# Kernel optimization log

Hardware: AMD Instinct MI355X
Metric: run time of the kernel (lower is better)

The kernel has to match this reference:

```python
import jax, jax.numpy as jnp
import numpy as np

B, S, D, H = 512, 512, 64, 128  # batch, seq_len, input_size, hidden_size


def setup_inputs() -> dict:
    key = jax.random.key(0)
    ks = jax.random.split(key, 12)
    s_in = 1.0 / np.sqrt(H)
    def u(k, shape):
        return jax.random.uniform(k, shape, jnp.float32, -s_in, s_in)
    return {
        "x": jax.random.normal(ks[0], (B, S, D), jnp.float32),
        # layer 0 (PyTorch gate order i,f,g,o stacked along first dim)
        "W_ih0": u(ks[1], (4 * H, D)),
        "W_hh0": u(ks[2], (4 * H, H)),
        "b_ih0": u(ks[3], (4 * H,)),
        "b_hh0": u(ks[4], (4 * H,)),
        # layer 1
        "W_ih1": u(ks[5], (4 * H, H)),
        "W_hh1": u(ks[6], (4 * H, H)),
        "b_ih1": u(ks[7], (4 * H,)),
        "b_hh1": u(ks[8], (4 * H,)),
        # linear head hidden -> 1
        "W_lin": u(ks[9], (1, H)),
        "b_lin": u(ks[10], (1,)),
    }


def _lstm_layer(x, W_ih, W_hh, b_ih, b_hh):
    # x: [B, S, Din] -> h sequence [B, S, H]
    b, s, _ = x.shape
    h_dim = W_hh.shape[1]
    # precompute input contribution for all timesteps (the compute-heavy GEMM)
    pre = jnp.einsum('bsd,gd->bsg', x, W_ih) + (b_ih + b_hh)  # [B, S, 4H]

    def step(carry, p_t):
        h, c = carry
        gates = p_t + h @ W_hh.T  # [B, 4H]
        i, f, g, o = jnp.split(gates, 4, axis=-1)
        i = jax.nn.sigmoid(i)
        f = jax.nn.sigmoid(f)
        g = jnp.tanh(g)
        o = jax.nn.sigmoid(o)
        c = f * c + i * g
        h = o * jnp.tanh(c)
        return (h, c), h

    h0 = jnp.zeros((b, h_dim), x.dtype)
    (_, _), hs = jax.lax.scan(step, (h0, h0), pre.transpose(1, 0, 2))
    return hs.transpose(1, 0, 2)  # [B, S, H]


def reference(x, W_ih0, W_hh0, b_ih0, b_hh0, W_ih1, W_hh1, b_ih1, b_hh1, W_lin, b_lin):
    h1 = _lstm_layer(x, W_ih0, W_hh0, b_ih0, b_hh0)
    h2 = _lstm_layer(h1, W_ih1, W_hh1, b_ih1, b_hh1)
    last = h2[:, -1, :]  # [B, H]
    return last @ W_lin.T + b_lin  # [B, 1]
```

## Files before the change

### kernel.cpp

```cpp
#include <hip/hip_runtime.h>

typedef _Float16 half8 __attribute__((ext_vector_type(8)));
typedef _Float16 half4 __attribute__((ext_vector_type(4)));
typedef _Float16 half2v __attribute__((ext_vector_type(2)));
typedef float floatx4 __attribute__((ext_vector_type(4)));

__device__ __forceinline__ float fast_rcp(float x) { return __builtin_amdgcn_rcpf(x); }
__device__ __forceinline__ float fast_sigmoid(float x) {
  return fast_rcp(1.f + __expf(-x));
}
__device__ __forceinline__ float fast_tanh(float x) {
  return 1.f - 2.f * fast_rcp(1.f + __expf(2.f * x));
}

__global__ void prep_kernel(const float* __restrict__ wih0, const float* __restrict__ whh0,
                            const float* __restrict__ bih0, const float* __restrict__ bhh0,
                            const float* __restrict__ wih1, const float* __restrict__ whh1,
                            const float* __restrict__ bih1, const float* __restrict__ bhh1,
                            _Float16* __restrict__ w0f, _Float16* __restrict__ w1f,
                            float* __restrict__ bias0, float* __restrict__ bias1)
{
  int stride = gridDim.x * blockDim.x;
  int idx0 = blockIdx.x * blockDim.x + threadIdx.x;
  const int N0 = 6*32*64*8;
  const int N1 = 8*32*64*8;
  for (int e = idx0; e < N0 + N1 + 1024; e += stride) {
    if (e < N0) {
      int j = e & 7; int le = e >> 3; int lane = le & 63; int frag = le >> 6;
      int kt = frag >> 5, ntile = frag & 31;
      int n = ntile*16 + (lane & 15);
      int kk = kt*32 + ((lane >> 4) << 3) + j;
      float v = (kk < 64) ? wih0[n*64 + kk] : whh0[n*128 + (kk - 64)];
      w0f[e] = (_Float16)v;
    } else if (e < N0 + N1) {
      int e2 = e - N0;
      int j = e2 & 7; int le = e2 >> 3; int lane = le & 63; int frag = le >> 6;
      int kt = frag >> 5, ntile = frag & 31;
      int n = ntile*16 + (lane & 15);
      int kk = kt*32 + ((lane >> 4) << 3) + j;
      float v = (kk < 128) ? wih1[n*128 + kk] : whh1[n*128 + (kk - 128)];
      w1f[e2] = (_Float16)v;
    } else {
      int i = e - (N0 + N1);
      if (i < 512) bias0[i] = bih0[i] + bhh0[i];
      else         bias1[i - 512] = bih1[i - 512] + bhh1[i - 512];
    }
  }
}


__global__ __launch_bounds__(512, 2) void lstm_l0(const float* __restrict__ x,
    const _Float16* __restrict__ w0f, const float* __restrict__ bias0,
    _Float16* __restrict__ h1out)
{
  const int tid = threadIdx.x;
  const int lane = tid & 63;
  const int w = tid >> 6;
  const int r0 = blockIdx.x * 2;

  __shared__ float preLDS[2][8192];
  __shared__ half8 aF[2][2*64];
  __shared__ half8 hA[2][4*8];
  __shared__ _Float16 hist[16][2][128];

  for (int i = tid; i < 2*4*8*4; i += 512) ((int*)hA)[i] = 0;

  half8 bf[6][4];
#pragma unroll
  for (int kt = 0; kt < 6; ++kt)
#pragma unroll
    for (int g = 0; g < 4; ++g) {
      int frag = kt*32 + (g*8 + w);
      bf[kt][g] = *reinterpret_cast<const half8*>(w0f + (size_t)(frag*64 + lane)*8);
      asm volatile("" : "+a"(bf[kt][g]));
    }
  float bias_v[4];
#pragma unroll
  for (int g = 0; g < 4; ++g) bias_v[g] = bias0[g*128 + w*16 + (lane & 15)];

  const int sdt = tid >> 6, sr = (tid >> 5) & 1, scp = (tid & 31) * 2;
  const int sm = sdt*2 + sr;
  const int sidx = ((scp>>5)*64 + sm + (((scp&31)>>3)<<4))*8 + (scp & 7);

  const bool arow = (lane & 11) == 0;
  const int cIdx = ((lane >> 4) << 1) | ((lane >> 2) & 1);
  const int rb = lane >> 4;
  const int en = w*16 + (lane & 15);
  const int eoff = ((en>>5)*8 + ((en&31)>>3)*2 + rb)*8 + (en&7);
  float cst = 0.f;

  {
    float2 v0 = *reinterpret_cast<const float2*>(x + ((size_t)(r0+sr)*512 + sdt)*64 + scp);
    float2 v1 = *reinterpret_cast<const float2*>(x + ((size_t)(r0+sr)*512 + 8 + sdt)*64 + scp);
    half2v h0; h0[0] = (_Float16)v0.x; h0[1] = (_Float16)v0.y;
    half2v h1v; h1v[0] = (_Float16)v1.x; h1v[1] = (_Float16)v1.y;
    *reinterpret_cast<half2v*>(((_Float16*)aF[0]) + sidx) = h0;
    *reinterpret_cast<half2v*>(((_Float16*)aF[1]) + sidx) = h1v;
  }
  __syncthreads();
  {
    floatx4 accP[4];
#pragma unroll
    for (int g = 0; g < 4; ++g) { float bb = bias_v[g]; accP[g] = (floatx4){bb,bb,bb,bb}; }
#pragma unroll
    for (int kt = 0; kt < 2; ++kt) {
      half8 af = aF[0][kt*64 + lane];
#pragma unroll
      for (int g = 0; g < 4; ++g)
        accP[g] = __builtin_amdgcn_mfma_f32_16x16x32_f16(af, bf[kt][g], accP[g], 0, 0, 0);
    }
#pragma unroll
    for (int reg = 0; reg < 4; ++reg) {
      int m = ((lane>>4)<<2) + reg;
      floatx4 pv = (floatx4){accP[0][reg], accP[1][reg], accP[2][reg], accP[3][reg]};
      *reinterpret_cast<floatx4*>(&preLDS[0][(m*128 + en)*4]) = pv;
    }
  }
  __syncthreads();

  half8 a2 = {}, a3 = {}, a4 = {}, a5 = {};

  for (int t = 0; t < 512; ++t) {
    const int b = t >> 3;
    if ((t & 7) == 0 && b < 62) {
      int s = (b+2)*8 + sdt;
      float2 v = *reinterpret_cast<const float2*>(x + ((size_t)(r0+sr)*512 + s)*64 + scp);
      half2v hv; hv[0] = (_Float16)v.x; hv[1] = (_Float16)v.y;
      *reinterpret_cast<half2v*>(((_Float16*)aF[b&1]) + sidx) = hv;
    }
    __syncthreads();
    if ((t & 7) == 0) {
      if (t != 0) {
        int tbase = t - 8;
        int fr = tid >> 8, rest = tid & 255;
        int fdt = rest >> 5, n = (rest & 31) * 4;
        half4 v = *reinterpret_cast<const half4*>(&hist[(tbase + fdt) & 15][fr][n]);
        *reinterpret_cast<half4*>(h1out + ((size_t)(r0 + fr)*512 + tbase + fdt)*128 + n) = v;
      }
      if (b < 63) {
        int slot = (b+1) & 1;
        floatx4 accP[4];
#pragma unroll
        for (int g = 0; g < 4; ++g) { float bb = bias_v[g]; accP[g] = (floatx4){bb,bb,bb,bb}; }
#pragma unroll
        for (int kt = 0; kt < 2; ++kt) {
          half8 af = aF[slot][kt*64 + lane];
#pragma unroll
          for (int g = 0; g < 4; ++g)
            accP[g] = __builtin_amdgcn_mfma_f32_16x16x32_f16(af, bf[kt][g], accP[g], 0, 0, 0);
        }
#pragma unroll
        for (int reg = 0; reg < 4; ++reg) {
          int m = ((lane>>4)<<2) + reg;
          floatx4 pv = (floatx4){accP[0][reg], accP[1][reg], accP[2][reg], accP[3][reg]};
          *reinterpret_cast<floatx4*>(&preLDS[slot][(m*128 + en)*4]) = pv;
        }
      }
    }

    floatx4 p4 = (floatx4){0.f, 0.f, 0.f, 0.f};
    if (lane < 32) {
      int mstep = ((t & 7) << 1) + rb;
      p4 = *reinterpret_cast<const floatx4*>(&preLDS[b & 1][(mstep*128 + en)*4]);
    }
    floatx4 acc[4];
#pragma unroll
    for (int g = 0; g < 4; ++g) acc[g] = (floatx4){p4[g], 0.f, 0.f, 0.f};

    const int cur = t & 1;
    if (arow) {
      a2 = hA[cur][0*8 + cIdx];
      a3 = hA[cur][1*8 + cIdx];
      a4 = hA[cur][2*8 + cIdx];
      a5 = hA[cur][3*8 + cIdx];
    }
#pragma unroll
    for (int g = 0; g < 4; ++g)
      acc[g] = __builtin_amdgcn_mfma_f32_16x16x32_f16(a2, bf[2][g], acc[g], 0, 0, 0);
#pragma unroll
    for (int g = 0; g < 4; ++g)
      acc[g] = __builtin_amdgcn_mfma_f32_16x16x32_f16(a3, bf[3][g], acc[g], 0, 0, 0);
#pragma unroll
    for (int g = 0; g < 4; ++g)
      acc[g] = __builtin_amdgcn_mfma_f32_16x16x32_f16(a4, bf[4][g], acc[g], 0, 0, 0);
#pragma unroll
    for (int g = 0; g < 4; ++g)
      acc[g] = __builtin_amdgcn_mfma_f32_16x16x32_f16(a5, bf[5][g], acc[g], 0, 0, 0);

    if (lane < 32) {
      float ii = fast_sigmoid(acc[0][0]);
      float ff = fast_sigmoid(acc[1][0]);
      float gg = fast_tanh(acc[2][0]);
      float oo = fast_sigmoid(acc[3][0]);
      cst = ff*cst + ii*gg;
      float hv2 = oo*fast_tanh(cst);
      _Float16 hh = (_Float16)hv2;
      ((_Float16*)hA[cur^1])[eoff] = hh;
      hist[t & 15][rb][en] = hh;
    }
  }
  __syncthreads();
  {
    int tbase = 504;
    int fr = tid >> 8, rest = tid & 255;
    int fdt = rest >> 5, n = (rest & 31) * 4;
    half4 v = *reinterpret_cast<const half4*>(&hist[(tbase + fdt) & 15][fr][n]);
    *reinterpret_cast<half4*>(h1out + ((size_t)(r0 + fr)*512 + tbase + fdt)*128 + n) = v;
  }
}

__global__ __launch_bounds__(512, 2) void lstm_l1(const _Float16* __restrict__ h1in,
    const _Float16* __restrict__ w1f, const float* __restrict__ bias1,
    const float* __restrict__ wlin, const float* __restrict__ blin,
    float* __restrict__ out)
{
  const int tid = threadIdx.x;
  const int lane = tid & 63;
  const int w = tid >> 6;
  const int r0 = blockIdx.x * 2;

  __shared__ float preLDS[2][8192];
  __shared__ half8 aF[2][4*64];
  __shared__ half8 hA[2][4*8];
  __shared__ float head[256];

  for (int i = tid; i < 2*4*8*4; i += 512) ((int*)hA)[i] = 0;

  half8 bf[8][4];
#pragma unroll
  for (int kt = 0; kt < 8; ++kt)
#pragma unroll
    for (int g = 0; g < 4; ++g) {
      int frag = kt*32 + (g*8 + w);
      bf[kt][g] = *reinterpret_cast<const half8*>(w1f + (size_t)(frag*64 + lane)*8);
      asm volatile("" : "+a"(bf[kt][g]));
    }
  float bias_v[4];
#pragma unroll
  for (int g = 0; g < 4; ++g) bias_v[g] = bias1[g*128 + w*16 + (lane & 15)];

  const int sdt = tid >> 6, sr = (tid >> 5) & 1, scq = (tid & 31) * 4;
  const int sm = sdt*2 + sr;
  const int sidx = ((scq>>5)*64 + sm + (((scq&31)>>3)<<4))*8 + (scq & 7);

  const bool arow = (lane & 11) == 0;
  const int cIdx = ((lane >> 4) << 1) | ((lane >> 2) & 1);
  const int rb = lane >> 4;
  const int en = w*16 + (lane & 15);
  const int eoff = ((en>>5)*8 + ((en&31)>>3)*2 + rb)*8 + (en&7);
  const float wl = (lane < 32) ? wlin[en] : 0.f;
  float cst = 0.f;
  float hl = 0.f;

  {
    uint2 v0 = *reinterpret_cast<const uint2*>(h1in + ((size_t)(r0+sr)*512 + sdt)*128 + scq);
    uint2 v1 = *reinterpret_cast<const uint2*>(h1in + ((size_t)(r0+sr)*512 + 8 + sdt)*128 + scq);
    *reinterpret_cast<uint2*>(((_Float16*)aF[0]) + sidx) = v0;
    *reinterpret_cast<uint2*>(((_Float16*)aF[1]) + sidx) = v1;
  }
  __syncthreads();
  {
    floatx4 accP[4];
#pragma unroll
    for (int g = 0; g < 4; ++g) { float bb = bias_v[g]; accP[g] = (floatx4){bb,bb,bb,bb}; }
#pragma unroll
    for (int kt = 0; kt < 4; ++kt) {
      half8 af = aF[0][kt*64 + lane];
#pragma unroll
      for (int g = 0; g < 4; ++g)
        accP[g] = __builtin_amdgcn_mfma_f32_16x16x32_f16(af, bf[kt][g], accP[g], 0, 0, 0);
    }
#pragma unroll
    for (int reg = 0; reg < 4; ++reg) {
      int m = ((lane>>4)<<2) + reg;
      floatx4 pv = (floatx4){accP[0][reg], accP[1][reg], accP[2][reg], accP[3][reg]};
      *reinterpret_cast<floatx4*>(&preLDS[0][(m*128 + en)*4]) = pv;
    }
  }
  __syncthreads();

  half8 a4 = {}, a5 = {}, a6 = {}, a7 = {};

  for (int t = 0; t < 512; ++t) {
    const int b = t >> 3;
    if ((t & 7) == 0 && b < 62) {
      int s = (b+2)*8 + sdt;
      uint2 v = *reinterpret_cast<const uint2*>(h1in + ((size_t)(r0+sr)*512 + s)*128 + scq);
      *reinterpret_cast<uint2*>(((_Float16*)aF[b&1]) + sidx) = v;
    }
    __syncthreads();
    if ((t & 7) == 0 && b < 63) {
      int slot = (b+1) & 1;
      floatx4 accP[4];
#pragma unroll
      for (int g = 0; g < 4; ++g) { float bb = bias_v[g]; accP[g] = (floatx4){bb,bb,bb,bb}; }
#pragma unroll
      for (int kt = 0; kt < 4; ++kt) {
        half8 af = aF[slot][kt*64 + lane];
#pragma unroll
        for (int g = 0; g < 4; ++g)
          accP[g] = __builtin_amdgcn_mfma_f32_16x16x32_f16(af, bf[kt][g], accP[g], 0, 0, 0);
      }
#pragma unroll
      for (int reg = 0; reg < 4; ++reg) {
        int m = ((lane>>4)<<2) + reg;
        floatx4 pv = (floatx4){accP[0][reg], accP[1][reg], accP[2][reg], accP[3][reg]};
        *reinterpret_cast<floatx4*>(&preLDS[slot][(m*128 + en)*4]) = pv;
      }
    }

    floatx4 p4 = (floatx4){0.f, 0.f, 0.f, 0.f};
    if (lane < 32) {
      int mstep = ((t & 7) << 1) + rb;
      p4 = *reinterpret_cast<const floatx4*>(&preLDS[b & 1][(mstep*128 + en)*4]);
    }
    floatx4 acc[4];
#pragma unroll
    for (int g = 0; g < 4; ++g) acc[g] = (floatx4){p4[g], 0.f, 0.f, 0.f};

    const int cur = t & 1;
    if (arow) {
      a4 = hA[cur][0*8 + cIdx];
      a5 = hA[cur][1*8 + cIdx];
      a6 = hA[cur][2*8 + cIdx];
      a7 = hA[cur][3*8 + cIdx];
    }
#pragma unroll
    for (int g = 0; g < 4; ++g)
      acc[g] = __builtin_amdgcn_mfma_f32_16x16x32_f16(a4, bf[4][g], acc[g], 0, 0, 0);
#pragma unroll
    for (int g = 0; g < 4; ++g)
      acc[g] = __builtin_amdgcn_mfma_f32_16x16x32_f16(a5, bf[5][g], acc[g], 0, 0, 0);
#pragma unroll
    for (int g = 0; g < 4; ++g)
      acc[g] = __builtin_amdgcn_mfma_f32_16x16x32_f16(a6, bf[6][g], acc[g], 0, 0, 0);
#pragma unroll
    for (int g = 0; g < 4; ++g)
      acc[g] = __builtin_amdgcn_mfma_f32_16x16x32_f16(a7, bf[7][g], acc[g], 0, 0, 0);

    if (lane < 32) {
      float ii = fast_sigmoid(acc[0][0]);
      float ff = fast_sigmoid(acc[1][0]);
      float gg = fast_tanh(acc[2][0]);
      float oo = fast_sigmoid(acc[3][0]);
      cst = ff*cst + ii*gg;
      hl = oo*fast_tanh(cst);
      ((_Float16*)hA[cur^1])[eoff] = (_Float16)hl;
    }
  }

  if (lane < 32) head[rb*128 + en] = hl * wl;
  __syncthreads();
  if (tid < 2) {
    float s = blin[0];
    for (int n = 0; n < 128; ++n) s += head[tid*128 + n];
    out[r0 + tid] = s;
  }
}

extern "C" void kernel_launch(void* const* d_in, const int* in_sizes, int n_in,
                              void* d_out, int out_size, void* d_ws, size_t ws_size,
                              hipStream_t stream)
{
  const float* x    = (const float*)d_in[0];
  const float* wih0 = (const float*)d_in[1];
  const float* whh0 = (const float*)d_in[2];
  const float* bih0 = (const float*)d_in[3];
  const float* bhh0 = (const float*)d_in[4];
  const float* wih1 = (const float*)d_in[5];
  const float* whh1 = (const float*)d_in[6];
  const float* bih1 = (const float*)d_in[7];
  const float* bhh1 = (const float*)d_in[8];
  const float* wlin = (const float*)d_in[9];
  const float* blin = (const float*)d_in[10];
  float* out = (float*)d_out;

  char* ws = (char*)d_ws;
  _Float16* w0f = (_Float16*)(ws);
  _Float16* w1f = (_Float16*)(ws + 196608);
  float* bias0  = (float*)(ws + 458752);
  float* bias1  = (float*)(ws + 460800);
  _Float16* h1  = (_Float16*)(ws + 1048576);

  prep_kernel<<<256, 256, 0, stream>>>(wih0, whh0, bih0, bhh0, wih1, whh1, bih1, bhh1,
                                       w0f, w1f, bias0, bias1);
  lstm_l0<<<256, 512, 0, stream>>>(x, w0f, bias0, h1);
  lstm_l1<<<256, 512, 0, stream>>>(h1, w1f, bias1, wlin, blin, out);
}
```

Measured before the change: 785.2 us.

## Fuse both LSTM layers into one wavefront-pipelined kernel

Merges the layer-0 and layer-1 kernels into a single kernel that runs layer 1 sixteen timesteps behind layer 0. Layer-0 outputs pass through an LDS history ring instead of a global h1 buffer. This removes the global round trip of h1 and the second launch, and lets the two recurrences interleave to hide latency. To fit registers, only the recurrent weights stay resident; the input-projection weights are reloaded from global memory every 8 steps. The cost is higher register and LDS pressure and a longer serial step per iteration.

```diff
diff --git a/kernel.cpp b/kernel.cpp
--- a/kernel.cpp
+++ b/kernel.cpp
@@ -48,168 +48,8 @@
   }
 }
 
-
-__global__ __launch_bounds__(512, 2) void lstm_l0(const float* __restrict__ x,
+__global__ __launch_bounds__(512, 2) void lstm_fused(const float* __restrict__ x,
     const _Float16* __restrict__ w0f, const float* __restrict__ bias0,
-    _Float16* __restrict__ h1out)
-{
-  const int tid = threadIdx.x;
-  const int lane = tid & 63;
-  const int w = tid >> 6;
-  const int r0 = blockIdx.x * 2;
-
-  __shared__ float preLDS[2][8192];
-  __shared__ half8 aF[2][2*64];
-  __shared__ half8 hA[2][4*8];
-  __shared__ _Float16 hist[16][2][128];
-
-  for (int i = tid; i < 2*4*8*4; i += 512) ((int*)hA)[i] = 0;
-
-  half8 bf[6][4];
-#pragma unroll
-  for (int kt = 0; kt < 6; ++kt)
-#pragma unroll
-    for (int g = 0; g < 4; ++g) {
-      int frag = kt*32 + (g*8 + w);
-      bf[kt][g] = *reinterpret_cast<const half8*>(w0f + (size_t)(frag*64 + lane)*8);
-      asm volatile("" : "+a"(bf[kt][g]));
-    }
-  float bias_v[4];
-#pragma unroll
-  for (int g = 0; g < 4; ++g) bias_v[g] = bias0[g*128 + w*16 + (lane & 15)];
-
-  const int sdt = tid >> 6, sr = (tid >> 5) & 1, scp = (tid & 31) * 2;
-  const int sm = sdt*2 + sr;
-  const int sidx = ((scp>>5)*64 + sm + (((scp&31)>>3)<<4))*8 + (scp & 7);
-
-  const bool arow = (lane & 11) == 0;
-  const int cIdx = ((lane >> 4) << 1) | ((lane >> 2) & 1);
-  const int rb = lane >> 4;
-  const int en = w*16 + (lane & 15);
-  const int eoff = ((en>>5)*8 + ((en&31)>>3)*2 + rb)*8 + (en&7);
-  float cst = 0.f;
-
-  {
-    float2 v0 = *reinterpret_cast<const float2*>(x + ((size_t)(r0+sr)*512 + sdt)*64 + scp);
-    float2 v1 = *reinterpret_cast<const float2*>(x + ((size_t)(r0+sr)*512 + 8 + sdt)*64 + scp);
-    half2v h0; h0[0] = (_Float16)v0.x; h0[1] = (_Float16)v0.y;
-    half2v h1v; h1v[0] = (_Float16)v1.x; h1v[1] = (_Float16)v1.y;
-    *reinterpret_cast<half2v*>(((_Float16*)aF[0]) + sidx) = h0;
-    *reinterpret_cast<half2v*>(((_Float16*)aF[1]) + sidx) = h1v;
-  }
-  __syncthreads();
-  {
-    floatx4 accP[4];
-#pragma unroll
-    for (int g = 0; g < 4; ++g) { float bb = bias_v[g]; accP[g] = (floatx4){bb,bb,bb,bb}; }
-#pragma unroll
-    for (int kt = 0; kt < 2; ++kt) {
-      half8 af = aF[0][kt*64 + lane];
-#pragma unroll
-      for (int g = 0; g < 4; ++g)
-        accP[g] = __builtin_amdgcn_mfma_f32_16x16x32_f16(af, bf[kt][g], accP[g], 0, 0, 0);
-    }
-#pragma unroll
-    for (int reg = 0; reg < 4; ++reg) {
-      int m = ((lane>>4)<<2) + reg;
-      floatx4 pv = (floatx4){accP[0][reg], accP[1][reg], accP[2][reg], accP[3][reg]};
-      *reinterpret_cast<floatx4*>(&preLDS[0][(m*128 + en)*4]) = pv;
-    }
-  }
-  __syncthreads();
-
-  half8 a2 = {}, a3 = {}, a4 = {}, a5 = {};
-
-  for (int t = 0; t < 512; ++t) {
-    const int b = t >> 3;
-    if ((t & 7) == 0 && b < 62) {
-      int s = (b+2)*8 + sdt;
-      float2 v = *reinterpret_cast<const float2*>(x + ((size_t)(r0+sr)*512 + s)*64 + scp);
-      half2v hv; hv[0] = (_Float16)v.x; hv[1] = (_Float16)v.y;
-      *reinterpret_cast<half2v*>(((_Float16*)aF[b&1]) + sidx) = hv;
-    }
-    __syncthreads();
-    if ((t & 7) == 0) {
-      if (t != 0) {
-        int tbase = t - 8;
-        int fr = tid >> 8, rest = tid & 255;
-        int fdt = rest >> 5, n = (rest & 31) * 4;
-        half4 v = *reinterpret_cast<const half4*>(&hist[(tbase + fdt) & 15][fr][n]);
-        *reinterpret_cast<half4*>(h1out + ((size_t)(r0 + fr)*512 + tbase + fdt)*128 + n) = v;
-      }
-      if (b < 63) {
-        int slot = (b+1) & 1;
-        floatx4 accP[4];
-#pragma unroll
-        for (int g = 0; g < 4; ++g) { float bb = bias_v[g]; accP[g] = (floatx4){bb,bb,bb,bb}; }
-#pragma unroll
-        for (int kt = 0; kt < 2; ++kt) {
-          half8 af = aF[slot][kt*64 + lane];
-#pragma unroll
-          for (int g = 0; g < 4; ++g)
-            accP[g] = __builtin_amdgcn_mfma_f32_16x16x32_f16(af, bf[kt][g], accP[g], 0, 0, 0);
-        }
-#pragma unroll
-        for (int reg = 0; reg < 4; ++reg) {
-          int m = ((lane>>4)<<2) + reg;
-          floatx4 pv = (floatx4){accP[0][reg], accP[1][reg], accP[2][reg], accP[3][reg]};
-          *reinterpret_cast<floatx4*>(&preLDS[slot][(m*128 + en)*4]) = pv;
-        }
-      }
-    }
-
-    floatx4 p4 = (floatx4){0.f, 0.f, 0.f, 0.f};
-    if (lane < 32) {
-      int mstep = ((t & 7) << 1) + rb;
-      p4 = *reinterpret_cast<const floatx4*>(&preLDS[b & 1][(mstep*128 + en)*4]);
-    }
-    floatx4 acc[4];
-#pragma unroll
-    for (int g = 0; g < 4; ++g) acc[g] = (floatx4){p4[g], 0.f, 0.f, 0.f};
-
-    const int cur = t & 1;
-    if (arow) {
-      a2 = hA[cur][0*8 + cIdx];
-      a3 = hA[cur][1*8 + cIdx];
-      a4 = hA[cur][2*8 + cIdx];
-      a5 = hA[cur][3*8 + cIdx];
-    }
-#pragma unroll
-    for (int g = 0; g < 4; ++g)
-      acc[g] = __builtin_amdgcn_mfma_f32_16x16x32_f16(a2, bf[2][g], acc[g], 0, 0, 0);
-#pragma unroll
-    for (int g = 0; g < 4; ++g)
-      acc[g] = __builtin_amdgcn_mfma_f32_16x16x32_f16(a3, bf[3][g], acc[g], 0, 0, 0);
-#pragma unroll
-    for (int g = 0; g < 4; ++g)
-      acc[g] = __builtin_amdgcn_mfma_f32_16x16x32_f16(a4, bf[4][g], acc[g], 0, 0, 0);
-#pragma unroll
-    for (int g = 0; g < 4; ++g)
-      acc[g] = __builtin_amdgcn_mfma_f32_16x16x32_f16(a5, bf[5][g], acc[g], 0, 0, 0);
-
-    if (lane < 32) {
-      float ii = fast_sigmoid(acc[0][0]);
-      float ff = fast_sigmoid(acc[1][0]);
-      float gg = fast_tanh(acc[2][0]);
-      float oo = fast_sigmoid(acc[3][0]);
-      cst = ff*cst + ii*gg;
-      float hv2 = oo*fast_tanh(cst);
-      _Float16 hh = (_Float16)hv2;
-      ((_Float16*)hA[cur^1])[eoff] = hh;
-      hist[t & 15][rb][en] = hh;
-    }
-  }
-  __syncthreads();
-  {
-    int tbase = 504;
-    int fr = tid >> 8, rest = tid & 255;
-    int fdt = rest >> 5, n = (rest & 31) * 4;
-    half4 v = *reinterpret_cast<const half4*>(&hist[(tbase + fdt) & 15][fr][n]);
-    *reinterpret_cast<half4*>(h1out + ((size_t)(r0 + fr)*512 + tbase + fdt)*128 + n) = v;
-  }
-}
-
-__global__ __launch_bounds__(512, 2) void lstm_l1(const _Float16* __restrict__ h1in,
     const _Float16* __restrict__ w1f, const float* __restrict__ bias1,
     const float* __restrict__ wlin, const float* __restrict__ blin,
     float* __restrict__ out)
@@ -219,29 +59,36 @@
   const int w = tid >> 6;
   const int r0 = blockIdx.x * 2;
 
-  __shared__ float preLDS[2][8192];
-  __shared__ half8 aF[2][4*64];
-  __shared__ half8 hA[2][4*8];
+  __shared__ float pre0[2][8192];
+  __shared__ float pre1[2][8192];
+  __shared__ half8 aF[2][2*64];
+  __shared__ half8 hA0[2][4*8];
+  __shared__ half8 hA1[2][4*8];
+  __shared__ _Float16 hist[16][2][128];
   __shared__ float head[256];
 
-  for (int i = tid; i < 2*4*8*4; i += 512) ((int*)hA)[i] = 0;
-
-  half8 bf[8][4];
-#pragma unroll
-  for (int kt = 0; kt < 8; ++kt)
+  if (tid < 256) { ((int*)hA0)[tid] = 0; ((int*)hA1)[tid] = 0; }
+
+  half8 bf0r[4][4], bf1r[4][4];
+#pragma unroll
+  for (int kt = 0; kt < 4; ++kt)
 #pragma unroll
     for (int g = 0; g < 4; ++g) {
-      int frag = kt*32 + (g*8 + w);
-      bf[kt][g] = *reinterpret_cast<const half8*>(w1f + (size_t)(frag*64 + lane)*8);
-      asm volatile("" : "+a"(bf[kt][g]));
-    }
-  float bias_v[4];
-#pragma unroll
-  for (int g = 0; g < 4; ++g) bias_v[g] = bias1[g*128 + w*16 + (lane & 15)];
-
-  const int sdt = tid >> 6, sr = (tid >> 5) & 1, scq = (tid & 31) * 4;
+      bf0r[kt][g] = *reinterpret_cast<const half8*>(w0f + (size_t)(((kt+2)*32 + g*8 + w)*64 + lane)*8);
+      asm volatile("" : "+a"(bf0r[kt][g]));
+      bf1r[kt][g] = *reinterpret_cast<const half8*>(w1f + (size_t)(((kt+4)*32 + g*8 + w)*64 + lane)*8);
+      asm volatile("" : "+a"(bf1r[kt][g]));
+    }
+  float b0v[4], b1v[4];
+#pragma unroll
+  for (int g = 0; g < 4; ++g) {
+    b0v[g] = bias0[g*128 + w*16 + (lane & 15)];
+    b1v[g] = bias1[g*128 + w*16 + (lane & 15)];
+  }
+
+  const int sdt = tid >> 6, sr = (tid >> 5) & 1, scp = (tid & 31) * 2;
   const int sm = sdt*2 + sr;
-  const int sidx = ((scq>>5)*64 + sm + (((scq&31)>>3)<<4))*8 + (scq & 7);
+  const int sidx = ((scp>>5)*64 + sm + (((scp&31)>>3)<<4))*8 + (scp & 7);
 
   const bool arow = (lane & 11) == 0;
   const int cIdx = ((lane >> 4) << 1) | ((lane >> 2) & 1);
@@ -249,103 +96,189 @@
   const int en = w*16 + (lane & 15);
   const int eoff = ((en>>5)*8 + ((en&31)>>3)*2 + rb)*8 + (en&7);
   const float wl = (lane < 32) ? wlin[en] : 0.f;
-  float cst = 0.f;
-  float hl = 0.f;
+  float cst0 = 0.f, cst1 = 0.f, hl = 0.f;
+
+  const int dtL = (lane & 15) >> 1;
+  const int rL  = lane & 1;
+  const int kbase = (lane >> 4) * 8;
 
   {
-    uint2 v0 = *reinterpret_cast<const uint2*>(h1in + ((size_t)(r0+sr)*512 + sdt)*128 + scq);
-    uint2 v1 = *reinterpret_cast<const uint2*>(h1in + ((size_t)(r0+sr)*512 + 8 + sdt)*128 + scq);
-    *reinterpret_cast<uint2*>(((_Float16*)aF[0]) + sidx) = v0;
-    *reinterpret_cast<uint2*>(((_Float16*)aF[1]) + sidx) = v1;
+    float2 v0 = *reinterpret_cast<const float2*>(x + ((size_t)(r0+sr)*512 + sdt)*64 + scp);
+    float2 v1 = *reinterpret_cast<const float2*>(x + ((size_t)(r0+sr)*512 + 8 + sdt)*64 + scp);
+    half2v h0; h0[0] = (_Float16)v0.x; h0[1] = (_Float16)v0.y;
+    half2v h1v; h1v[0] = (_Float16)v1.x; h1v[1] = (_Float16)v1.y;
+    *reinterpret_cast<half2v*>(((_Float16*)aF[0]) + sidx) = h0;
+    *reinterpret_cast<half2v*>(((_Float16*)aF[1]) + sidx) = h1v;
   }
   __syncthreads();
   {
     floatx4 accP[4];
 #pragma unroll
-    for (int g = 0; g < 4; ++g) { float bb = bias_v[g]; accP[g] = (floatx4){bb,bb,bb,bb}; }
-#pragma unroll
-    for (int kt = 0; kt < 4; ++kt) {
+    for (int g = 0; g < 4; ++g) { float bb = b0v[g]; accP[g] = (floatx4){bb,bb,bb,bb}; }
+#pragma unroll
+    for (int kt = 0; kt < 2; ++kt) {
       half8 af = aF[0][kt*64 + lane];
 #pragma unroll
-      for (int g = 0; g < 4; ++g)
-        accP[g] = __builtin_amdgcn_mfma_f32_16x16x32_f16(af, bf[kt][g], accP[g], 0, 0, 0);
+      for (int g = 0; g < 4; ++g) {
+        half8 wf = *reinterpret_cast<const half8*>(w0f + (size_t)((kt*32 + g*8 + w)*64 + lane)*8);
+        accP[g] = __builtin_amdgcn_mfma_f32_16x16x32_f16(af, wf, accP[g], 0, 0, 0);
+      }
     }
 #pragma unroll
     for (int reg = 0; reg < 4; ++reg) {
       int m = ((lane>>4)<<2) + reg;
       floatx4 pv = (floatx4){accP[0][reg], accP[1][reg], accP[2][reg], accP[3][reg]};
-      *reinterpret_cast<floatx4*>(&preLDS[0][(m*128 + en)*4]) = pv;
+      *reinterpret_cast<floatx4*>(&pre0[0][(m*128 + en)*4]) = pv;
     }
   }
   __syncthreads();
 
-  half8 a4 = {}, a5 = {}, a6 = {}, a7 = {};
-
-  for (int t = 0; t < 512; ++t) {
-    const int b = t >> 3;
-    if ((t & 7) == 0 && b < 62) {
+  half8 a00 = {}, a01 = {}, a02 = {}, a03 = {};
+  half8 a10 = {}, a11 = {}, a12 = {}, a13 = {};
+
+  for (int p = 0; p < 528; ++p) {
+    const int b = p >> 3;
+    if ((p & 7) == 0 && b < 62) {
       int s = (b+2)*8 + sdt;
-      uint2 v = *reinterpret_cast<const uint2*>(h1in + ((size_t)(r0+sr)*512 + s)*128 + scq);
-      *reinterpret_cast<uint2*>(((_Float16*)aF[b&1]) + sidx) = v;
+      float2 v = *reinterpret_cast<const float2*>(x + ((size_t)(r0+sr)*512 + s)*64 + scp);
+      half2v hv; hv[0] = (_Float16)v.x; hv[1] = (_Float16)v.y;
+      *reinterpret_cast<half2v*>(((_Float16*)aF[b&1]) + sidx) = hv;
     }
     __syncthreads();
-    if ((t & 7) == 0 && b < 63) {
-      int slot = (b+1) & 1;
-      floatx4 accP[4];
-#pragma unroll
-      for (int g = 0; g < 4; ++g) { float bb = bias_v[g]; accP[g] = (floatx4){bb,bb,bb,bb}; }
-#pragma unroll
-      for (int kt = 0; kt < 4; ++kt) {
-        half8 af = aF[slot][kt*64 + lane];
-#pragma unroll
-        for (int g = 0; g < 4; ++g)
-          accP[g] = __builtin_amdgcn_mfma_f32_16x16x32_f16(af, bf[kt][g], accP[g], 0, 0, 0);
-      }
-#pragma unroll
-      for (int reg = 0; reg < 4; ++reg) {
-        int m = ((lane>>4)<<2) + reg;
-        floatx4 pv = (floatx4){accP[0][reg], accP[1][reg], accP[2][reg], accP[3][reg]};
-        *reinterpret_cast<floatx4*>(&preLDS[slot][(m*128 + en)*4]) = pv;
-      }
-    }
-
-    floatx4 p4 = (floatx4){0.f, 0.f, 0.f, 0.f};
-    if (lane < 32) {
-      int mstep = ((t & 7) << 1) + rb;
-      p4 = *reinterpret_cast<const floatx4*>(&preLDS[b & 1][(mstep*128 + en)*4]);
-    }
-    floatx4 acc[4];
-#pragma unroll
-    for (int g = 0; g < 4; ++g) acc[g] = (floatx4){p4[g], 0.f, 0.f, 0.f};
-
-    const int cur = t & 1;
-    if (arow) {
-      a4 = hA[cur][0*8 + cIdx];
-      a5 = hA[cur][1*8 + cIdx];
-      a6 = hA[cur][2*8 + cIdx];
-      a7 = hA[cur][3*8 + cIdx];
-    }
-#pragma unroll
-    for (int g = 0; g < 4; ++g)
-      acc[g] = __builtin_amdgcn_mfma_f32_16x16x32_f16(a4, bf[4][g], acc[g], 0, 0, 0);
-#pragma unroll
-    for (int g = 0; g < 4; ++g)
-      acc[g] = __builtin_amdgcn_mfma_f32_16x16x32_f16(a5, bf[5][g], acc[g], 0, 0, 0);
-#pragma unroll
-    for (int g = 0; g < 4; ++g)
-      acc[g] = __builtin_amdgcn_mfma_f32_16x16x32_f16(a6, bf[6][g], acc[g], 0, 0, 0);
-#pragma unroll
-    for (int g = 0; g < 4; ++g)
-      acc[g] = __builtin_amdgcn_mfma_f32_16x16x32_f16(a7, bf[7][g], acc[g], 0, 0, 0);
-
-    if (lane < 32) {
-      float ii = fast_sigmoid(acc[0][0]);
-      float ff = fast_sigmoid(acc[1][0]);
-      float gg = fast_tanh(acc[2][0]);
-      float oo = fast_sigmoid(acc[3][0]);
-      cst = ff*cst + ii*gg;
-      hl = oo*fast_tanh(cst);
-      ((_Float16*)hA[cur^1])[eoff] = (_Float16)hl;
+
+    if ((p & 7) == 0) {
+      const _Float16* w0p = w0f; asm volatile("" : "+v"(w0p));
+      const _Float16* w1p = w1f; asm volatile("" : "+v"(w1p));
+      if (b < 63) {
+        int slot = (b+1) & 1;
+        floatx4 accP[4];
+#pragma unroll
+        for (int g = 0; g < 4; ++g) { float bb2 = b0v[g]; accP[g] = (floatx4){bb2,bb2,bb2,bb2}; }
+#pragma unroll
+        for (int kt = 0; kt < 2; ++kt) {
+          half8 af = aF[slot][kt*64 + lane];
+#pragma unroll
+          for (int g = 0; g < 4; ++g) {
+            half8 wf = *reinterpret_cast<const half8*>(w0p + (size_t)((kt*32 + g*8 + w)*64 + lane)*8);
+            accP[g] = __builtin_amdgcn_mfma_f32_16x16x32_f16(af, wf, accP[g], 0, 0, 0);
+          }
+        }
+#pragma unroll
+        for (int reg = 0; reg < 4; ++reg) {
+          int m = ((lane>>4)<<2) + reg;
+          floatx4 pv = (floatx4){accP[0][reg], accP[1][reg], accP[2][reg], accP[3][reg]};
+          *reinterpret_cast<floatx4*>(&pre0[slot][(m*128 + en)*4]) = pv;
+        }
+      }
+      int bb = b - 1;
+      if (bb >= 0 && bb < 64) {
+        int slot = bb & 1;
+        const _Float16* hrow = &hist[(bb & 1)*8 + dtL][rL][kbase];
+        floatx4 accP[4];
+#pragma unroll
+        for (int g = 0; g < 4; ++g) { float bb2 = b1v[g]; accP[g] = (floatx4){bb2,bb2,bb2,bb2}; }
+#pragma unroll
+        for (int kt = 0; kt < 4; ++kt) {
+          half8 af = *reinterpret_cast<const half8*>(hrow + kt*32);
+#pragma unroll
+          for (int g = 0; g < 4; ++g) {
+            half8 wf = *reinterpret_cast<const half8*>(w1p + (size_t)((kt*32 + g*8 + w)*64 + lane)*8);
+            accP[g] = __builtin_amdgcn_mfma_f32_16x16x32_f16(af, wf, accP[g], 0, 0, 0);
+          }
+        }
+#pragma unroll
+        for (int reg = 0; reg < 4; ++reg) {
+          int m = ((lane>>4)<<2) + reg;
+          floatx4 pv = (floatx4){accP[0][reg], accP[1][reg], accP[2][reg], accP[3][reg]};
+          *reinterpret_cast<floatx4*>(&pre1[slot][(m*128 + en)*4]) = pv;
+        }
+      }
+    }
+
+    if (p < 512) {
+      floatx4 p4 = (floatx4){0.f, 0.f, 0.f, 0.f};
+      if (lane < 32) {
+        int mstep = ((p & 7) << 1) + rb;
+        p4 = *reinterpret_cast<const floatx4*>(&pre0[b & 1][(mstep*128 + en)*4]);
+      }
+      floatx4 acc[4];
+#pragma unroll
+      for (int g = 0; g < 4; ++g) acc[g] = (floatx4){p4[g], 0.f, 0.f, 0.f};
+
+      const int cur = p & 1;
+      if (arow) {
+        a00 = hA0[cur][0*8 + cIdx];
+        a01 = hA0[cur][1*8 + cIdx];
+        a02 = hA0[cur][2*8 + cIdx];
+        a03 = hA0[cur][3*8 + cIdx];
+      }
+#pragma unroll
+      for (int g = 0; g < 4; ++g)
+        acc[g] = __builtin_amdgcn_mfma_f32_16x16x32_f16(a00, bf0r[0][g], acc[g], 0, 0, 0);
+#pragma unroll
+      for (int g = 0; g < 4; ++g)
+        acc[g] = __builtin_amdgcn_mfma_f32_16x16x32_f16(a01, bf0r[1][g], acc[g], 0, 0, 0);
+#pragma unroll
+      for (int g = 0; g < 4; ++g)
+        acc[g] = __builtin_amdgcn_mfma_f32_16x16x32_f16(a02, bf0r[2][g], acc[g], 0, 0, 0);
+#pragma unroll
+      for (int g = 0; g < 4; ++g)
+        acc[g] = __builtin_amdgcn_mfma_f32_16x16x32_f16(a03, bf0r[3][g], acc[g], 0, 0, 0);
+
+      if (lane < 32) {
+        float ii = fast_sigmoid(acc[0][0]);
+        float ff = fast_sigmoid(acc[1][0]);
+        float gg = fast_tanh(acc[2][0]);
+        float oo = fast_sigmoid(acc[3][0]);
+        cst0 = ff*cst0 + ii*gg;
+        float hv2 = oo*fast_tanh(cst0);
+        _Float16 hh = (_Float16)hv2;
+        ((_Float16*)hA0[cur^1])[eoff] = hh;
+        hist[p & 15][rb][en] = hh;
+      }
+    }
+
+    if (p >= 16) {
+      const int t1 = p - 16;
+      const int b1 = t1 >> 3;
+      floatx4 p4 = (floatx4){0.f, 0.f, 0.f, 0.f};
+      if (lane < 32) {
+        int mstep = ((t1 & 7) << 1) + rb;
+        p4 = *reinterpret_cast<const floatx4*>(&pre1[b1 & 1][(mstep*128 + en)*4]);
+      }
+      floatx4 acc[4];
+#pragma unroll
+      for (int g = 0; g < 4; ++g) acc[g] = (floatx4){p4[g], 0.f, 0.f, 0.f};
+
+      const int cur = t1 & 1;
+      if (arow) {
+        a10 = hA1[cur][0*8 + cIdx];
+        a11 = hA1[cur][1*8 + cIdx];
+        a12 = hA1[cur][2*8 + cIdx];
+        a13 = hA1[cur][3*8 + cIdx];
+      }
+#pragma unroll
+      for (int g = 0; g < 4; ++g)
+        acc[g] = __builtin_amdgcn_mfma_f32_16x16x32_f16(a10, bf1r[0][g], acc[g], 0, 0, 0);
+#pragma unroll
+      for (int g = 0; g < 4; ++g)
+        acc[g] = __builtin_amdgcn_mfma_f32_16x16x32_f16(a11, bf1r[1][g], acc[g], 0, 0, 0);
+#pragma unroll
+      for (int g = 0; g < 4; ++g)
+        acc[g] = __builtin_amdgcn_mfma_f32_16x16x32_f16(a12, bf1r[2][g], acc[g], 0, 0, 0);
+#pragma unroll
+      for (int g = 0; g < 4; ++g)
+        acc[g] = __builtin_amdgcn_mfma_f32_16x16x32_f16(a13, bf1r[3][g], acc[g], 0, 0, 0);
+
+      if (lane < 32) {
+        float ii = fast_sigmoid(acc[0][0]);
+        float ff = fast_sigmoid(acc[1][0]);
+        float gg = fast_tanh(acc[2][0]);
+        float oo = fast_sigmoid(acc[3][0]);
+        cst1 = ff*cst1 + ii*gg;
+        hl = oo*fast_tanh(cst1);
+        ((_Float16*)hA1[cur^1])[eoff] = (_Float16)hl;
+      }
     }
   }
 
@@ -380,10 +313,8 @@
   _Float16* w1f = (_Float16*)(ws + 196608);
   float* bias0  = (float*)(ws + 458752);
   float* bias1  = (float*)(ws + 460800);
-  _Float16* h1  = (_Float16*)(ws + 1048576);
 
   prep_kernel<<<256, 256, 0, stream>>>(wih0, whh0, bih0, bhh0, wih1, whh1, bih1, bhh1,
                                        w0f, w1f, bias0, bias1);
-  lstm_l0<<<256, 512, 0, stream>>>(x, w0f, bias0, h1);
-  lstm_l1<<<256, 512, 0, stream>>>(h1, w1f, bias1, wlin, blin, out);
-}
+  lstm_fused<<<256, 512, 0, stream>>>(x, w0f, bias0, w1f, bias1, wlin, blin, out);
+}
```

Result: slower. 889.3 us (+13.3%).

## Spread per-block prefetch, input GEMM and history stores across timestep phases

Applied to the files above, without the earlier changes.

The work that used to run every eighth timestep (global load of the next input chunk, the input-projection MFMAs and the history write-back) is now split across several phases of the 8-step block. The global load is issued at phase 0 and consumed at phase 1, and the projection is split over phases 2 and 3. The preactivation for the next step is read from LDS right after the recurrent MFMAs, so its latency is off the critical path. This is meant to smooth out the per-step latency spikes of the serial recurrence, at the cost of more live registers and phase-dependent branches.

```diff
diff --git a/kernel.cpp b/kernel.cpp
--- a/kernel.cpp
+++ b/kernel.cpp
@@ -48,7 +48,6 @@
   }
 }
 
-
 __global__ __launch_bounds__(512, 2) void lstm_l0(const float* __restrict__ x,
     const _Float16* __restrict__ w0f, const float* __restrict__ bias0,
     _Float16* __restrict__ h1out)
@@ -99,73 +98,78 @@
   }
   __syncthreads();
   {
-    floatx4 accP[4];
-#pragma unroll
-    for (int g = 0; g < 4; ++g) { float bb = bias_v[g]; accP[g] = (floatx4){bb,bb,bb,bb}; }
+    floatx4 accP0[4];
+#pragma unroll
+    for (int g = 0; g < 4; ++g) { float bb = bias_v[g]; accP0[g] = (floatx4){bb,bb,bb,bb}; }
 #pragma unroll
     for (int kt = 0; kt < 2; ++kt) {
       half8 af = aF[0][kt*64 + lane];
 #pragma unroll
       for (int g = 0; g < 4; ++g)
-        accP[g] = __builtin_amdgcn_mfma_f32_16x16x32_f16(af, bf[kt][g], accP[g], 0, 0, 0);
+        accP0[g] = __builtin_amdgcn_mfma_f32_16x16x32_f16(af, bf[kt][g], accP0[g], 0, 0, 0);
     }
 #pragma unroll
     for (int reg = 0; reg < 4; ++reg) {
       int m = ((lane>>4)<<2) + reg;
-      floatx4 pv = (floatx4){accP[0][reg], accP[1][reg], accP[2][reg], accP[3][reg]};
+      floatx4 pv = (floatx4){accP0[0][reg], accP0[1][reg], accP0[2][reg], accP0[3][reg]};
       *reinterpret_cast<floatx4*>(&preLDS[0][(m*128 + en)*4]) = pv;
     }
   }
-  __syncthreads();
 
   half8 a2 = {}, a3 = {}, a4 = {}, a5 = {};
+  float2 sv;
+  floatx4 accP[4];
+  floatx4 acc[4];
+#pragma unroll
+  for (int g = 0; g < 4; ++g) { acc[g] = (floatx4){0.f,0.f,0.f,0.f}; accP[g] = acc[g]; }
+
+  floatx4 p4c = (floatx4){0.f,0.f,0.f,0.f};
+  if (lane < 32)
+    p4c = *reinterpret_cast<const floatx4*>(&preLDS[0][(rb*128 + en)*4]);
 
   for (int t = 0; t < 512; ++t) {
     const int b = t >> 3;
-    if ((t & 7) == 0 && b < 62) {
+    __syncthreads();
+    const int ph = t & 7;
+    if (ph == 0 && b < 62) {
       int s = (b+2)*8 + sdt;
-      float2 v = *reinterpret_cast<const float2*>(x + ((size_t)(r0+sr)*512 + s)*64 + scp);
-      half2v hv; hv[0] = (_Float16)v.x; hv[1] = (_Float16)v.y;
+      sv = *reinterpret_cast<const float2*>(x + ((size_t)(r0+sr)*512 + s)*64 + scp);
+    }
+    if (ph == 1 && b < 62) {
+      half2v hv; hv[0] = (_Float16)sv.x; hv[1] = (_Float16)sv.y;
       *reinterpret_cast<half2v*>(((_Float16*)aF[b&1]) + sidx) = hv;
     }
-    __syncthreads();
-    if ((t & 7) == 0) {
-      if (t != 0) {
-        int tbase = t - 8;
-        int fr = tid >> 8, rest = tid & 255;
-        int fdt = rest >> 5, n = (rest & 31) * 4;
-        half4 v = *reinterpret_cast<const half4*>(&hist[(tbase + fdt) & 15][fr][n]);
-        *reinterpret_cast<half4*>(h1out + ((size_t)(r0 + fr)*512 + tbase + fdt)*128 + n) = v;
+    if (ph == 2 && b < 63) {
+      int slot = (b+1) & 1;
+#pragma unroll
+      for (int g = 0; g < 4; ++g) { float bb = bias_v[g]; accP[g] = (floatx4){bb,bb,bb,bb}; }
+      half8 af = aF[slot][lane];
+#pragma unroll
+      for (int g = 0; g < 4; ++g)
+        accP[g] = __builtin_amdgcn_mfma_f32_16x16x32_f16(af, bf[0][g], accP[g], 0, 0, 0);
+    }
+    if (ph == 3 && b < 63) {
+      int slot = (b+1) & 1;
+      half8 af = aF[slot][64 + lane];
+#pragma unroll
+      for (int g = 0; g < 4; ++g)
+        accP[g] = __builtin_amdgcn_mfma_f32_16x16x32_f16(af, bf[1][g], accP[g], 0, 0, 0);
+#pragma unroll
+      for (int reg = 0; reg < 4; ++reg) {
+        int m = ((lane>>4)<<2) + reg;
+        floatx4 pv = (floatx4){accP[0][reg], accP[1][reg], accP[2][reg], accP[3][reg]};
+        *reinterpret_cast<floatx4*>(&preLDS[slot][(m*128 + en)*4]) = pv;
       }
-      if (b < 63) {
-        int slot = (b+1) & 1;
-        floatx4 accP[4];
-#pragma unroll
-        for (int g = 0; g < 4; ++g) { float bb = bias_v[g]; accP[g] = (floatx4){bb,bb,bb,bb}; }
-#pragma unroll
-        for (int kt = 0; kt < 2; ++kt) {
-          half8 af = aF[slot][kt*64 + lane];
-#pragma unroll
-          for (int g = 0; g < 4; ++g)
-            accP[g] = __builtin_amdgcn_mfma_f32_16x16x32_f16(af, bf[kt][g], accP[g], 0, 0, 0);
-        }
-#pragma unroll
-        for (int reg = 0; reg < 4; ++reg) {
-          int m = ((lane>>4)<<2) + reg;
-          floatx4 pv = (floatx4){accP[0][reg], accP[1][reg], accP[2][reg], accP[3][reg]};
-          *reinterpret_cast<floatx4*>(&preLDS[slot][(m*128 + en)*4]) = pv;
-        }
-      }
-    }
-
-    floatx4 p4 = (floatx4){0.f, 0.f, 0.f, 0.f};
-    if (lane < 32) {
-      int mstep = ((t & 7) << 1) + rb;
-      p4 = *reinterpret_cast<const floatx4*>(&preLDS[b & 1][(mstep*128 + en)*4]);
-    }
-    floatx4 acc[4];
-#pragma unroll
-    for (int g = 0; g < 4; ++g) acc[g] = (floatx4){p4[g], 0.f, 0.f, 0.f};
+    }
+    if (ph == 5 && t >= 13) {
+      int tbase = t - 13;
+      int fr = tid >> 8, rest = tid & 255;
+      int fdt = rest >> 5, n = (rest & 31) * 4;
+      half4 v = *reinterpret_cast<const half4*>(&hist[(tbase + fdt) & 15][fr][n]);
+      *reinterpret_cast<half4*>(h1out + ((size_t)(r0 + fr)*512 + tbase + fdt)*128 + n) = v;
+    }
+
+    acc[0][0] = p4c[0]; acc[1][0] = p4c[1]; acc[2][0] = p4c[2]; acc[3][0] = p4c[3];
 
     const int cur = t & 1;
     if (arow) {
@@ -186,6 +190,12 @@
 #pragma unroll
     for (int g = 0; g < 4; ++g)
       acc[g] = __builtin_amdgcn_mfma_f32_16x16x32_f16(a5, bf[5][g], acc[g], 0, 0, 0);
+
+    if (lane < 32 && t < 511) {
+      int tn = t + 1;
+      int mstep = ((tn & 7) << 1) + rb;
+      p4c = *reinterpret_cast<const floatx4*>(&preLDS[(tn >> 3) & 1][(mstep*128 + en)*4]);
+    }
 
     if (lane < 32) {
       float ii = fast_sigmoid(acc[0][0]);
@@ -260,42 +270,62 @@
   }
   __syncthreads();
   {
-    floatx4 accP[4];
-#pragma unroll
-    for (int g = 0; g < 4; ++g) { float bb = bias_v[g]; accP[g] = (floatx4){bb,bb,bb,bb}; }
+    floatx4 accP0[4];
+#pragma unroll
+    for (int g = 0; g < 4; ++g) { float bb = bias_v[g]; accP0[g] = (floatx4){bb,bb,bb,bb}; }
 #pragma unroll
     for (int kt = 0; kt < 4; ++kt) {
       half8 af = aF[0][kt*64 + lane];
 #pragma unroll
       for (int g = 0; g < 4; ++g)
-        accP[g] = __builtin_amdgcn_mfma_f32_16x16x32_f16(af, bf[kt][g], accP[g], 0, 0, 0);
+        accP0[g] = __builtin_amdgcn_mfma_f32_16x16x32_f16(af, bf[kt][g], accP0[g], 0, 0, 0);
     }
 #pragma unroll
     for (int reg = 0; reg < 4; ++reg) {
       int m = ((lane>>4)<<2) + reg;
-      floatx4 pv = (floatx4){accP[0][reg], accP[1][reg], accP[2][reg], accP[3][reg]};
+      floatx4 pv = (floatx4){accP0[0][reg], accP0[1][reg], accP0[2][reg], accP0[3][reg]};
       *reinterpret_cast<floatx4*>(&preLDS[0][(m*128 + en)*4]) = pv;
     }
   }
-  __syncthreads();
 
   half8 a4 = {}, a5 = {}, a6 = {}, a7 = {};
+  uint2 sv;
+  floatx4 accP[4];
+  floatx4 acc[4];
+#pragma unroll
+  for (int g = 0; g < 4; ++g) { acc[g] = (floatx4){0.f,0.f,0.f,0.f}; accP[g] = acc[g]; }
+
+  floatx4 p4c = (floatx4){0.f,0.f,0.f,0.f};
+  if (lane < 32)
+    p4c = *reinterpret_cast<const floatx4*>(&preLDS[0][(rb*128 + en)*4]);
 
   for (int t = 0; t < 512; ++t) {
     const int b = t >> 3;
-    if ((t & 7) == 0 && b < 62) {
+    __syncthreads();
+    const int ph = t & 7;
+    if (ph == 0 && b < 62) {
       int s = (b+2)*8 + sdt;
-      uint2 v = *reinterpret_cast<const uint2*>(h1in + ((size_t)(r0+sr)*512 + s)*128 + scq);
-      *reinterpret_cast<uint2*>(((_Float16*)aF[b&1]) + sidx) = v;
-    }
-    __syncthreads();
-    if ((t & 7) == 0 && b < 63) {
+      sv = *reinterpret_cast<const uint2*>(h1in + ((size_t)(r0+sr)*512 + s)*128 + scq);
+    }
+    if (ph == 1 && b < 62) {
+      *reinterpret_cast<uint2*>(((_Float16*)aF[b&1]) + sidx) = sv;
+    }
+    if (ph == 2 && b < 63) {
       int slot = (b+1) & 1;
-      floatx4 accP[4];
 #pragma unroll
       for (int g = 0; g < 4; ++g) { float bb = bias_v[g]; accP[g] = (floatx4){bb,bb,bb,bb}; }
 #pragma unroll
-      for (int kt = 0; kt < 4; ++kt) {
+      for (int kt = 0; kt < 2; ++kt) {
+        half8 af = aF[slot][kt*64 + lane];
+#pragma unroll
+        for (int g = 0; g < 4; ++g)
+          accP[g] = __builtin_amdgcn_mfma_f32_16x16x32_f16(af, bf[kt][g], accP[g], 0, 0, 0);
+      }
+    }
+    if (ph == 3 && b < 63) {
+      int slot = (b+1) & 1;
+#pragma unroll
+      for (int kt = 2; kt < 4; ++kt) {
         half8 af = aF[slot][kt*64 + lane];
 #pragma unroll
         for (int g = 0; g < 4; ++g)
@@ -309,14 +339,7 @@
       }
     }
 
-    floatx4 p4 = (floatx4){0.f, 0.f, 0.f, 0.f};
-    if (lane < 32) {
-      int mstep = ((t & 7) << 1) + rb;
-      p4 = *reinterpret_cast<const floatx4*>(&preLDS[b & 1][(mstep*128 + en)*4]);
-    }
-    floatx4 acc[4];
-#pragma unroll
-    for (int g = 0; g < 4; ++g) acc[g] = (floatx4){p4[g], 0.f, 0.f, 0.f};
+    acc[0][0] = p4c[0]; acc[1][0] = p4c[1]; acc[2][0] = p4c[2]; acc[3][0] = p4c[3];
 
     const int cur = t & 1;
     if (arow) {
@@ -337,6 +360,12 @@
 #pragma unroll
     for (int g = 0; g < 4; ++g)
       acc[g] = __builtin_amdgcn_mfma_f32_16x16x32_f16(a7, bf[7][g], acc[g], 0, 0, 0);
+
+    if (lane < 32 && t < 511) {
+      int tn = t + 1;
+      int mstep = ((tn & 7) << 1) + rb;
+      p4c = *reinterpret_cast<const floatx4*>(&preLDS[(tn >> 3) & 1][(mstep*128 + en)*4]);
+    }
 
     if (lane < 32) {
       float ii = fast_sigmoid(acc[0][0]);
```

Measured after the change: 878.7 us. +11.9%, slower.
